# Performance work log

Measured on AMD Instinct MI355X. Metric: run time of the kernel, lower is better.

Reference implementation:

```python
import jax, jax.numpy as jnp
import numpy as np

N_NODES = 128   # num_nodes
BATCH = 4096
HIDDEN = 32     # fixed by the module's Linear(N+1, 32)


def setup_inputs() -> dict:
    key = jax.random.key(0)
    ks = jax.random.split(key, 8)
    N, B, H = N_NODES, BATCH, HIDDEN
    x = jax.random.normal(ks[0], (B, N), dtype=jnp.float32)
    # adjacency masks: A[b, :, j] = parent indicator of node j in sample b
    A = (jax.random.uniform(ks[1], (B, N, N)) < 0.3).astype(jnp.float32)
    # per-sample topological permutation
    order = jax.vmap(lambda k: jax.random.permutation(k, N))(
        jax.random.split(ks[2], B)).astype(jnp.int32)
    # intervention target per sample, -1 = no intervention
    do_idxs = jax.random.randint(ks[3], (B,), -1, N, dtype=jnp.int32)
    # externalized intervention noise (torch.normal in the original forward)
    u = jax.random.normal(ks[4], (B,), dtype=jnp.float32)
    # stacked per-node MLP params: Linear(N+1, 32) -> LeakyReLU -> Linear(32, 1)
    W1 = jax.random.normal(ks[5], (N, N + 1, H), dtype=jnp.float32) / np.sqrt(N + 1)
    b1 = jnp.zeros((N, H), dtype=jnp.float32)
    W2 = jax.random.normal(ks[6], (N, H, 1), dtype=jnp.float32) / np.sqrt(H)
    b2 = jnp.zeros((N, 1), dtype=jnp.float32)
    return dict(x=x, A=A, u=u, W1=W1, b1=b1, W2=W2, b2=b2,
                order=order, do_idxs=do_idxs)


def reference(x, A, u, W1, b1, W2, b2, order, do_idxs):
    B, N = x.shape
    bidx = jnp.arange(B)
    # set intervened entries: outputs[b, do_idxs[b]] = u[b] where do_idxs != -1
    outputs0 = jnp.where(do_idxs[:, None] == jnp.arange(N)[None, :],
                         u[:, None], jnp.zeros_like(x))

    def step(outputs, node):           # node: [B] current node per sample
        mask = A[bidx, :, node]        # [B, N] parent mask of this node
        ins = jnp.concatenate([mask * outputs,
                               x[bidx, node][:, None]], axis=1)  # [B, N+1]
        # per-node MLP gathered by node id (grouped tiny GEMMs)
        h = jax.nn.leaky_relu(jnp.einsum('bd,bdh->bh', ins, W1[node]) + b1[node])
        out = (jnp.einsum('bh,bho->bo', h, W2[node]) + b2[node])[:, 0]  # [B]
        # intervened samples keep their value u (they are skipped in the original)
        new_val = jnp.where(do_idxs == node, outputs[bidx, node], out)
        return outputs.at[bidx, node].set(new_val), None

    outputs, _ = jax.lax.scan(step, outputs0, order.T)  # sequential topo order
    return outputs
```

## Files before the change

### kernel.cpp

```cpp
#include <hip/hip_runtime.h>
#include <stdint.h>

#define NN 128
#define BB 4096
#define HH 32

__global__ __launch_bounds__(256) void pack_bits(const float* __restrict__ A,
                                                 unsigned long long* __restrict__ bitsW) {
    int t = blockIdx.x * 256 + threadIdx.x;
    int n4 = t & 31;
    int h  = (t >> 5) & 1;
    int b  = t >> 6;
    const float4* Ap = (const float4*)(A + (size_t)b * NN * NN + (size_t)h * 64 * NN) + n4;
    unsigned long long m0 = 0, m1 = 0, m2 = 0, m3 = 0;
#pragma unroll 8
    for (int d = 0; d < 64; ++d) {
        float4 v = Ap[(size_t)d * (NN / 4)];
        unsigned long long bit = 1ull << d;
        if (v.x != 0.f) m0 |= bit;
        if (v.y != 0.f) m1 |= bit;
        if (v.z != 0.f) m2 |= bit;
        if (v.w != 0.f) m3 |= bit;
    }
    unsigned long long* dst = bitsW + ((size_t)b * NN + n4 * 4) * 2 + h;
    dst[0] = m0; dst[2] = m1; dst[4] = m2; dst[6] = m3;
}

__global__ __launch_bounds__(128) void cond_mlp(
    const float* __restrict__ x, const float* __restrict__ u,
    const float* __restrict__ W1, const float* __restrict__ b1,
    const float* __restrict__ W2, const float* __restrict__ b2,
    const int* __restrict__ order, const int* __restrict__ do_idxs,
    const ulonglong2* __restrict__ bitsT, float* __restrict__ out)
{
    const int b = blockIdx.x;
    const int tid = threadIdx.x;
    const int lane = tid & 63;
    const int wv = tid >> 6;
    const int j = tid & 31;
    const int quarter = (tid >> 5) & 3;

    __shared__ float2 ent[132];
    __shared__ float part[2][32];

    const float ub = u[b];
    const int dob = do_idxs[b];
    float out0 = (dob == lane) ? ub : 0.f;
    float out1 = (dob == lane + 64) ? ub : 0.f;

    const int* ord = order + b * NN;
    const ulonglong2* bb = bitsT + (size_t)b * NN;

    int node = ord[0];
    ulonglong2 bits = bb[node];

    for (int t = 0; t < NN; ++t) {
        const int node_n = (t < NN - 1) ? ord[t + 1] : 0;
        const ulonglong2 bits_n = bb[node_n];

        const float* Wn = W1 + (size_t)node * (NN + 1) * HH;
        const float w2v = W2[node * HH + j];
        const float b1v = b1[node * HH + j];
        const float xv  = x[b * NN + node];
        const float b2v = b2[node];

        unsigned long long bal0 = __ballot(out0 != 0.f) & bits.x;
        unsigned long long bal1 = __ballot(out1 != 0.f) & bits.y;
        const int c0 = __popcll(bal0);
        const int cnt = c0 + __popcll(bal1);
        const int cnt4 = (cnt + 3) & ~3;
        if (wv == 0) {
            const unsigned long long below = (1ull << lane) - 1;
            if (bal0 & (1ull << lane)) {
                int p = __popcll(bal0 & below);
                ent[p] = make_float2(out0, __int_as_float(lane));
            }
            if (bal1 & (1ull << lane)) {
                int p = c0 + __popcll(bal1 & below);
                ent[p] = make_float2(out1, __int_as_float(lane + 64));
            }
            if (lane < cnt4 - cnt) ent[cnt + lane] = make_float2(0.f, __int_as_float(0));
        }
        __syncthreads();

        float acc = 0.f;
        for (int k = quarter; k < cnt4; k += 4) {
            float2 e = ent[k];
            acc += e.x * Wn[__float_as_int(e.y) * HH + j];
        }
        acc += __shfl_xor(acc, 32);
        if (lane < 32) part[wv][j] = acc;
        __syncthreads();

        float acc2 = acc + part[1 - wv][j];
        acc2 += xv * Wn[NN * HH + j];
        acc2 += b1v;
        const float hv = (acc2 > 0.f) ? acc2 : 0.01f * acc2;

        float p = hv * w2v;
        p += __shfl_xor(p, 16);
        p += __shfl_xor(p, 8);
        p += __shfl_xor(p, 4);
        p += __shfl_xor(p, 2);
        p += __shfl_xor(p, 1);
        const float outv = p + b2v;

        if (dob != node) {
            if (lane == (node & 63)) {
                if (node < 64) out0 = outv; else out1 = outv;
            }
        }
        node = node_n;
        bits = bits_n;
    }

    if (wv == 0) {
        out[b * NN + lane] = out0;
        out[b * NN + 64 + lane] = out1;
    }
}

extern "C" void kernel_launch(void* const* d_in, const int* in_sizes, int n_in,
                              void* d_out, int out_size, void* d_ws, size_t ws_size,
                              hipStream_t stream) {
    const float* x   = (const float*)d_in[0];
    const float* A   = (const float*)d_in[1];
    const float* u   = (const float*)d_in[2];
    const float* W1  = (const float*)d_in[3];
    const float* b1  = (const float*)d_in[4];
    const float* W2  = (const float*)d_in[5];
    const float* b2  = (const float*)d_in[6];
    const int* order = (const int*)d_in[7];
    const int* dox   = (const int*)d_in[8];

    unsigned long long* bitsW = (unsigned long long*)d_ws;

    pack_bits<<<(BB * 64) / 256, 256, 0, stream>>>(A, bitsW);
    cond_mlp<<<BB, 128, 0, stream>>>(x, u, W1, b1, W2, b2, order, dox,
                                     (const ulonglong2*)bitsW, (float*)d_out);
}
```

Baseline: 611.1 us.

## Use single-wave blocks with readlane broadcast instead of LDS compaction and barriers

Each sample now runs in one 64-lane wave instead of two waves. Active parent values are walked with ctz over the ballot masks and broadcast with readlane, so the LDS compaction buffer and both __syncthreads per step go away. The dot product uses four independent accumulators over pairs of set bits. The cost is that the serial loop work falls on one wave, which halves per-block parallelism for the gathered W1 loads, and the readlane lane indices must be uniform scalars.

```diff
diff --git a/kernel.cpp b/kernel.cpp
--- a/kernel.cpp
+++ b/kernel.cpp
@@ -26,7 +26,12 @@
     dst[0] = m0; dst[2] = m1; dst[4] = m2; dst[6] = m3;
 }
 
-__global__ __launch_bounds__(128) void cond_mlp(
+__device__ __forceinline__ float bcast_lane(float v, int lane) {
+    return __uint_as_float(
+        (unsigned)__builtin_amdgcn_readlane((int)__float_as_uint(v), lane));
+}
+
+__global__ __launch_bounds__(64) void cond_mlp(
     const float* __restrict__ x, const float* __restrict__ u,
     const float* __restrict__ W1, const float* __restrict__ b1,
     const float* __restrict__ W2, const float* __restrict__ b2,
@@ -34,14 +39,8 @@
     const ulonglong2* __restrict__ bitsT, float* __restrict__ out)
 {
     const int b = blockIdx.x;
-    const int tid = threadIdx.x;
-    const int lane = tid & 63;
-    const int wv = tid >> 6;
-    const int j = tid & 31;
-    const int quarter = (tid >> 5) & 3;
-
-    __shared__ float2 ent[132];
-    __shared__ float part[2][32];
+    const int lane = threadIdx.x;
+    const int j = lane & 31;
 
     const float ub = u[b];
     const int dob = do_idxs[b];
@@ -58,44 +57,49 @@
         const int node_n = (t < NN - 1) ? ord[t + 1] : 0;
         const ulonglong2 bits_n = bb[node_n];
 
-        const float* Wn = W1 + (size_t)node * (NN + 1) * HH;
+        const float* __restrict__ Wn = W1 + (size_t)node * (NN + 1) * HH;
         const float w2v = W2[node * HH + j];
         const float b1v = b1[node * HH + j];
+        const float wxv = Wn[NN * HH + j];
         const float xv  = x[b * NN + node];
         const float b2v = b2[node];
 
-        unsigned long long bal0 = __ballot(out0 != 0.f) & bits.x;
-        unsigned long long bal1 = __ballot(out1 != 0.f) & bits.y;
-        const int c0 = __popcll(bal0);
-        const int cnt = c0 + __popcll(bal1);
-        const int cnt4 = (cnt + 3) & ~3;
-        if (wv == 0) {
-            const unsigned long long below = (1ull << lane) - 1;
-            if (bal0 & (1ull << lane)) {
-                int p = __popcll(bal0 & below);
-                ent[p] = make_float2(out0, __int_as_float(lane));
+        unsigned long long m0 = __ballot(out0 != 0.f) & bits.x;
+        unsigned long long m1 = __ballot(out1 != 0.f) & bits.y;
+
+        float acc0 = 0.f, acc1 = 0.f, acc2 = 0.f, acc3 = 0.f;
+        while (m0 | m1) {
+            if (m0) {
+                int d0 = __builtin_ctzll(m0); m0 &= m0 - 1;
+                int d1 = 0; float v1 = 0.f;
+                if (m0) {
+                    d1 = __builtin_ctzll(m0); m0 &= m0 - 1;
+                    v1 = bcast_lane(out0, d1);
+                }
+                float v0 = bcast_lane(out0, d0);
+                float w0 = Wn[d0 * HH + j];
+                float w1 = Wn[d1 * HH + j];
+                acc0 = fmaf(v0, w0, acc0);
+                acc1 = fmaf(v1, w1, acc1);
             }
-            if (bal1 & (1ull << lane)) {
-                int p = c0 + __popcll(bal1 & below);
-                ent[p] = make_float2(out1, __int_as_float(lane + 64));
+            if (m1) {
+                int d0 = __builtin_ctzll(m1); m1 &= m1 - 1;
+                int d1 = 0; float v1 = 0.f;
+                if (m1) {
+                    d1 = __builtin_ctzll(m1); m1 &= m1 - 1;
+                    v1 = bcast_lane(out1, d1);
+                }
+                float v0 = bcast_lane(out1, d0);
+                float w0 = Wn[(64 + d0) * HH + j];
+                float w1 = Wn[(64 + d1) * HH + j];
+                acc2 = fmaf(v0, w0, acc2);
+                acc3 = fmaf(v1, w1, acc3);
             }
-            if (lane < cnt4 - cnt) ent[cnt + lane] = make_float2(0.f, __int_as_float(0));
         }
-        __syncthreads();
 
-        float acc = 0.f;
-        for (int k = quarter; k < cnt4; k += 4) {
-            float2 e = ent[k];
-            acc += e.x * Wn[__float_as_int(e.y) * HH + j];
-        }
-        acc += __shfl_xor(acc, 32);
-        if (lane < 32) part[wv][j] = acc;
-        __syncthreads();
-
-        float acc2 = acc + part[1 - wv][j];
-        acc2 += xv * Wn[NN * HH + j];
-        acc2 += b1v;
-        const float hv = (acc2 > 0.f) ? acc2 : 0.01f * acc2;
+        float acc = (acc0 + acc1) + (acc2 + acc3);
+        acc = fmaf(xv, wxv, acc) + b1v;
+        const float hv = fmaxf(acc, 0.01f * acc);
 
         float p = hv * w2v;
         p += __shfl_xor(p, 16);
@@ -114,10 +118,8 @@
         bits = bits_n;
     }
 
-    if (wv == 0) {
-        out[b * NN + lane] = out0;
-        out[b * NN + 64 + lane] = out1;
-    }
+    out[b * NN + lane] = out0;
+    out[b * NN + 64 + lane] = out1;
 }
 
 extern "C" void kernel_launch(void* const* d_in, const int* in_sizes, int n_in,
@@ -136,6 +138,6 @@
     unsigned long long* bitsW = (unsigned long long*)d_ws;
 
     pack_bits<<<(BB * 64) / 256, 256, 0, stream>>>(A, bitsW);
-    cond_mlp<<<BB, 128, 0, stream>>>(x, u, W1, b1, W2, b2, order, dox,
-                                     (const ulonglong2*)bitsW, (float*)d_out);
+    cond_mlp<<<BB, 64, 0, stream>>>(x, u, W1, b1, W2, b2, order, dox,
+                                    (const ulonglong2*)bitsW, (float*)d_out);
 }
```

Result: slower. 701.4 us (+14.8%).

## Precompute per-step active-parent lists from topological order and use single-wave kernel

Applied to the files above, without the earlier changes.

Adds a build_lists kernel that computes, for each sample and step, the set of parents already evaluated (prefix of the topological order plus the intervened node) intersected with the adjacency bits, and writes them as compact byte index lists. The main kernel then runs with one wavefront per sample, reading the precomputed list and doing the gathered dot products without per-step ballots, compaction or __syncthreads. The ballot fallback kernel is also collapsed to one wave. This removes the per-step synchronization and compaction from the serial loop, at the cost of an extra kernel, 32MB of workspace traffic and a dependence on workspace size.

```diff
diff --git a/kernel.cpp b/kernel.cpp
--- a/kernel.cpp
+++ b/kernel.cpp
@@ -26,7 +26,146 @@
     dst[0] = m0; dst[2] = m1; dst[4] = m2; dst[6] = m3;
 }
 
-__global__ __launch_bounds__(128) void cond_mlp(
+__device__ __forceinline__ void fill_slot(uint8_t* s, int node,
+                                          uint64_t m0, uint64_t m1) {
+    int cnt = __popcll(m0) + __popcll(m1);
+    s[1] = (uint8_t)node;
+    if (cnt <= 60) {
+        int c = 0;
+        while (m0) { int d = __builtin_ctzll(m0); m0 &= m0 - 1; s[4 + c] = (uint8_t)d; ++c; }
+        while (m1) { int d = __builtin_ctzll(m1); m1 &= m1 - 1; s[4 + c] = (uint8_t)(64 + d); ++c; }
+        while (c & 3) { s[4 + c] = 128; ++c; }
+        s[0] = (uint8_t)c;
+    } else {
+        s[0] = 255;
+        *(uint64_t*)(s + 8)  = m0;
+        *(uint64_t*)(s + 16) = m1;
+    }
+}
+
+__global__ __launch_bounds__(256) void build_lists(
+    const ulonglong2* __restrict__ bitsT, const int* __restrict__ order,
+    const int* __restrict__ do_idxs, uint8_t* __restrict__ lists)
+{
+    __shared__ uint8_t slot[4][128][64];
+    const int wv = threadIdx.x >> 6, lane = threadIdx.x & 63;
+    const int b = blockIdx.x * 4 + wv;
+    const int na  = order[b * NN + lane];
+    const int nb  = order[b * NN + 64 + lane];
+    const int dob = do_idxs[b];
+
+    uint64_t sa_lo = (na < 64) ? (1ull << na) : 0ull;
+    uint64_t sa_hi = (na < 64) ? 0ull : (1ull << (na - 64));
+    uint64_t sb_lo = (nb < 64) ? (1ull << nb) : 0ull;
+    uint64_t sb_hi = (nb < 64) ? 0ull : (1ull << (nb - 64));
+#pragma unroll
+    for (int s = 1; s < 64; s <<= 1) {
+        uint64_t t0 = __shfl_up(sa_lo, s), t1 = __shfl_up(sa_hi, s);
+        uint64_t t2 = __shfl_up(sb_lo, s), t3 = __shfl_up(sb_hi, s);
+        if (lane >= s) { sa_lo |= t0; sa_hi |= t1; sb_lo |= t2; sb_hi |= t3; }
+    }
+    uint64_t Pa_lo = __shfl_up(sa_lo, 1), Pa_hi = __shfl_up(sa_hi, 1);
+    uint64_t Pb_lo = __shfl_up(sb_lo, 1), Pb_hi = __shfl_up(sb_hi, 1);
+    if (lane == 0) { Pa_lo = 0; Pa_hi = 0; Pb_lo = 0; Pb_hi = 0; }
+    const uint64_t f_lo = __shfl(sa_lo, 63), f_hi = __shfl(sa_hi, 63);
+    Pb_lo |= f_lo; Pb_hi |= f_hi;
+    if (dob >= 0) {
+        uint64_t dlo = (dob < 64) ? (1ull << dob) : 0ull;
+        uint64_t dhi = (dob < 64) ? 0ull : (1ull << (dob - 64));
+        Pa_lo |= dlo; Pa_hi |= dhi; Pb_lo |= dlo; Pb_hi |= dhi;
+    }
+    const ulonglong2 ba = bitsT[(size_t)b * NN + na];
+    const ulonglong2 bc = bitsT[(size_t)b * NN + nb];
+    fill_slot(&slot[wv][lane][0],      na, Pa_lo & ba.x, Pa_hi & ba.y);
+    fill_slot(&slot[wv][64 + lane][0], nb, Pb_lo & bc.x, Pb_hi & bc.y);
+    __syncthreads();
+    const int4* src = (const int4*)&slot[0][0][0];
+    int4* dst = (int4*)(lists + (size_t)blockIdx.x * 32768);
+    for (int i = threadIdx.x; i < 2048; i += 256) dst[i] = src[i];
+}
+
+#define ENTB(w, sh) { int d = ((w) >> (sh)) & 255; \
+    const float* rp = Wn + d * HH; \
+    float wv = rp[j]; float vv = vals[d]; acc = fmaf(vv, wv, acc); }
+#define CHUNK(w) ENTB(w, 0) ENTB(w, 8) ENTB(w, 16) ENTB(w, 24)
+
+__global__ __launch_bounds__(64) void cond_mlp_list(
+    const float* __restrict__ x, const float* __restrict__ u,
+    const float* __restrict__ W1, const float* __restrict__ b1,
+    const float* __restrict__ W2, const float* __restrict__ b2,
+    const int* __restrict__ do_idxs, const uint8_t* __restrict__ lists,
+    float* __restrict__ out)
+{
+    const int b = blockIdx.x;
+    const int lane = threadIdx.x;
+    const int j = lane & 31;
+
+    __shared__ float vals[132];
+    const int dob = do_idxs[b];
+    const float ub = u[b];
+    vals[lane]      = (lane == dob) ? ub : 0.f;
+    vals[64 + lane] = (lane + 64 == dob) ? ub : 0.f;
+    if (lane < 4) vals[128 + lane] = 0.f;
+    __syncthreads();
+
+    const uint32_t* sp = (const uint32_t*)(lists + (size_t)b * 8192);
+
+    for (int t = 0; t < NN; ++t) {
+        const uint32_t* s = sp + (t << 4);
+        uint32_t h0 = s[0], h1 = s[1], h2 = s[2],  h3 = s[3];
+        uint32_t h4 = s[4], h5 = s[5], h6 = s[6],  h7 = s[7];
+        uint32_t h8 = s[8], h9 = s[9], h10 = s[10], h11 = s[11];
+        uint32_t h12 = s[12], h13 = s[13], h14 = s[14], h15 = s[15];
+        const int cnt  = h0 & 255;
+        const int node = (h0 >> 8) & 255;
+
+        const float* __restrict__ Wn = W1 + (size_t)node * (NN + 1) * HH;
+        const float w2v = W2[node * HH + j];
+        const float b1v = b1[node * HH + j];
+        const float wxv = Wn[NN * HH + j];
+        const float xv  = x[(b << 7) + node];
+        const float b2v = b2[node];
+
+        float acc = 0.f;
+        if (cnt != 255) {
+            switch (cnt >> 2) {
+            case 15: CHUNK(h15); case 14: CHUNK(h14); case 13: CHUNK(h13);
+            case 12: CHUNK(h12); case 11: CHUNK(h11); case 10: CHUNK(h10);
+            case 9:  CHUNK(h9);  case 8:  CHUNK(h8);  case 7:  CHUNK(h7);
+            case 6:  CHUNK(h6);  case 5:  CHUNK(h5);  case 4:  CHUNK(h4);
+            case 3:  CHUNK(h3);  case 2:  CHUNK(h2);  case 1:  CHUNK(h1);
+            case 0:  ;
+            }
+        } else {
+            uint64_t m0 = ((uint64_t)h3 << 32) | h2;
+            uint64_t m1 = ((uint64_t)h5 << 32) | h4;
+            while (m0) { int d = __builtin_ctzll(m0); m0 &= m0 - 1;
+                         acc = fmaf(vals[d], Wn[d * HH + j], acc); }
+            while (m1) { int d = __builtin_ctzll(m1); m1 &= m1 - 1;
+                         acc = fmaf(vals[64 + d], Wn[(64 + d) * HH + j], acc); }
+        }
+
+        acc = fmaf(xv, wxv, acc) + b1v;
+        const float hv = fmaxf(acc, 0.01f * acc);
+
+        float p = hv * w2v;
+        p += __shfl_xor(p, 16);
+        p += __shfl_xor(p, 8);
+        p += __shfl_xor(p, 4);
+        p += __shfl_xor(p, 2);
+        p += __shfl_xor(p, 1);
+        const float outv = p + b2v;
+
+        if (node != dob) {
+            if (lane == 0) vals[node] = outv;
+        }
+    }
+
+    out[b * NN + lane]      = vals[lane];
+    out[b * NN + 64 + lane] = vals[64 + lane];
+}
+
+__global__ __launch_bounds__(64) void cond_mlp_ballot(
     const float* __restrict__ x, const float* __restrict__ u,
     const float* __restrict__ W1, const float* __restrict__ b1,
     const float* __restrict__ W2, const float* __restrict__ b2,
@@ -34,14 +173,11 @@
     const ulonglong2* __restrict__ bitsT, float* __restrict__ out)
 {
     const int b = blockIdx.x;
-    const int tid = threadIdx.x;
-    const int lane = tid & 63;
-    const int wv = tid >> 6;
-    const int j = tid & 31;
-    const int quarter = (tid >> 5) & 3;
+    const int lane = threadIdx.x;
+    const int j = lane & 31;
+    const int half = lane >> 5;
 
     __shared__ float2 ent[132];
-    __shared__ float part[2][32];
 
     const float ub = u[b];
     const int dob = do_idxs[b];
@@ -68,34 +204,33 @@
         unsigned long long bal1 = __ballot(out1 != 0.f) & bits.y;
         const int c0 = __popcll(bal0);
         const int cnt = c0 + __popcll(bal1);
+        const unsigned long long below = (1ull << lane) - 1;
+        if (bal0 & (1ull << lane)) {
+            int p = __popcll(bal0 & below);
+            ent[p] = make_float2(out0, __int_as_float(lane));
+        }
+        if (bal1 & (1ull << lane)) {
+            int p = c0 + __popcll(bal1 & below);
+            ent[p] = make_float2(out1, __int_as_float(lane + 64));
+        }
         const int cnt4 = (cnt + 3) & ~3;
-        if (wv == 0) {
-            const unsigned long long below = (1ull << lane) - 1;
-            if (bal0 & (1ull << lane)) {
-                int p = __popcll(bal0 & below);
-                ent[p] = make_float2(out0, __int_as_float(lane));
-            }
-            if (bal1 & (1ull << lane)) {
-                int p = c0 + __popcll(bal1 & below);
-                ent[p] = make_float2(out1, __int_as_float(lane + 64));
-            }
-            if (lane < cnt4 - cnt) ent[cnt + lane] = make_float2(0.f, __int_as_float(0));
-        }
+        if (lane < cnt4 - cnt) ent[cnt + lane] = make_float2(0.f, __int_as_float(0));
         __syncthreads();
 
-        float acc = 0.f;
-        for (int k = quarter; k < cnt4; k += 4) {
-            float2 e = ent[k];
-            acc += e.x * Wn[__float_as_int(e.y) * HH + j];
-        }
+        float acc0 = 0.f, acc1 = 0.f;
+        for (int k = 0; k < cnt4; k += 4) {
+            float2 eA = ent[k + half];
+            float2 eB = ent[k + 2 + half];
+            acc0 += eA.x * Wn[__float_as_int(eA.y) * HH + j];
+            acc1 += eB.x * Wn[__float_as_int(eB.y) * HH + j];
+        }
+        __syncthreads();
+
+        float acc = acc0 + acc1;
         acc += __shfl_xor(acc, 32);
-        if (lane < 32) part[wv][j] = acc;
-        __syncthreads();
-
-        float acc2 = acc + part[1 - wv][j];
-        acc2 += xv * Wn[NN * HH + j];
-        acc2 += b1v;
-        const float hv = (acc2 > 0.f) ? acc2 : 0.01f * acc2;
+        acc += xv * Wn[NN * HH + j];
+        acc += b1v;
+        const float hv = (acc > 0.f) ? acc : 0.01f * acc;
 
         float p = hv * w2v;
         p += __shfl_xor(p, 16);
@@ -114,10 +249,8 @@
         bits = bits_n;
     }
 
-    if (wv == 0) {
-        out[b * NN + lane] = out0;
-        out[b * NN + 64 + lane] = out1;
-    }
+    out[b * NN + lane] = out0;
+    out[b * NN + 64 + lane] = out1;
 }
 
 extern "C" void kernel_launch(void* const* d_in, const int* in_sizes, int n_in,
@@ -134,8 +267,15 @@
     const int* dox   = (const int*)d_in[8];
 
     unsigned long long* bitsW = (unsigned long long*)d_ws;
+    uint8_t* lists = (uint8_t*)d_ws + (size_t)8 * 1024 * 1024;
+    const size_t need = (size_t)8 * 1024 * 1024 + (size_t)BB * NN * 64;
 
     pack_bits<<<(BB * 64) / 256, 256, 0, stream>>>(A, bitsW);
-    cond_mlp<<<BB, 128, 0, stream>>>(x, u, W1, b1, W2, b2, order, dox,
-                                     (const ulonglong2*)bitsW, (float*)d_out);
-}
+    if (ws_size >= need) {
+        build_lists<<<BB / 4, 256, 0, stream>>>((const ulonglong2*)bitsW, order, dox, lists);
+        cond_mlp_list<<<BB, 64, 0, stream>>>(x, u, W1, b1, W2, b2, dox, lists, (float*)d_out);
+    } else {
+        cond_mlp_ballot<<<BB, 64, 0, stream>>>(x, u, W1, b1, W2, b2, order, dox,
+                                               (const ulonglong2*)bitsW, (float*)d_out);
+    }
+}
```

New measurement: 663.5 us. 1.09x slower.
